# Kernel optimization log

Measured on AMD Instinct MI355X. Metric: run time of the kernel, lower is better.

The kernel has to match this reference:

```python
import jax, jax.numpy as jnp
import numpy as np

N_NODES = 100000
IN_CH = 256
EMBED = 256
N_EDGES = 300000
EPS = 1e-5


def _glorot(key, shape):
    fan_in, fan_out = shape[0], shape[1]
    lim = (6.0 / (fan_in + fan_out)) ** 0.5
    return jax.random.uniform(key, shape, jnp.float32, -lim, lim)


def setup_inputs() -> dict:
    key = jax.random.key(0)
    ks = jax.random.split(key, 16)
    inp = {}
    inp['node_feat'] = jax.random.normal(ks[0], (N_NODES, IN_CH), jnp.float32)
    inp['src'] = jax.random.randint(ks[1], (N_EDGES,), 0, N_NODES, jnp.int32)
    inp['dst'] = jax.random.randint(ks[2], (N_EDGES,), 0, N_NODES, jnp.int32)
    inp['neg'] = jax.random.randint(ks[3], (N_EDGES,), 0, N_NODES, jnp.int32)
    # GCNConv weights (x @ W + b), 3 layers
    inp['W1'] = _glorot(ks[4], (IN_CH, EMBED)); inp['b1'] = jnp.zeros((EMBED,), jnp.float32)
    inp['W2'] = _glorot(ks[5], (EMBED, EMBED)); inp['b2'] = jnp.zeros((EMBED,), jnp.float32)
    inp['W3'] = _glorot(ks[6], (EMBED, EMBED)); inp['b3'] = jnp.zeros((EMBED,), jnp.float32)
    # BatchNorm affine params (2 BN layers)
    inp['g1'] = jnp.ones((EMBED,), jnp.float32); inp['be1'] = jnp.zeros((EMBED,), jnp.float32)
    inp['g2'] = jnp.ones((EMBED,), jnp.float32); inp['be2'] = jnp.zeros((EMBED,), jnp.float32)
    # LinkPredictor MLP
    inp['fc1_w'] = _glorot(ks[7], (2 * EMBED, EMBED)); inp['fc1_b'] = jnp.zeros((EMBED,), jnp.float32)
    inp['fc2_w'] = _glorot(ks[8], (EMBED, 1)); inp['fc2_b'] = jnp.zeros((1,), jnp.float32)
    return inp


def gcn_conv(x, W, b, src, dst, n):
    # PyG GCNConv: out = D^{-1/2} (A + I) D^{-1/2} (x @ W) + b
    xw = x @ W
    loops = jnp.arange(n, dtype=src.dtype)
    src_l = jnp.concatenate([src, loops])
    dst_l = jnp.concatenate([dst, loops])
    deg = jax.ops.segment_sum(jnp.ones_like(dst_l, jnp.float32), dst_l, num_segments=n)
    dinv = jnp.where(deg > 0, jax.lax.rsqrt(deg), 0.0)
    norm = dinv[src_l] * dinv[dst_l]  # [E+N]
    msg = norm[:, None] * xw[src_l]   # [E+N, d]
    out = jax.ops.segment_sum(msg, dst_l, num_segments=n)
    return out + b


def batch_norm(x, g, b):
    # training-mode BN over node dim, biased variance (torch semantics)
    mu = jnp.mean(x, axis=0)
    var = jnp.mean((x - mu) ** 2, axis=0)
    return (x - mu) * jax.lax.rsqrt(var + EPS) * g + b


def link_pred(z_a, z_b, fc1_w, fc1_b, fc2_w, fc2_b):
    h = jnp.concatenate([z_a, z_b], axis=1) @ fc1_w + fc1_b
    h = jax.nn.relu(h)
    return jax.nn.sigmoid(h @ fc2_w + fc2_b).reshape(-1)


def reference(node_feat, src, dst, neg, W1, b1, W2, b2, W3, b3, g1, be1, g2, be2, fc1_w, fc1_b, fc2_w, fc2_b):
    n = node_feat.shape[0]
    # encoder (dropout p used only in training; inference/deterministic here)
    x = gcn_conv(node_feat, W1, b1, src, dst, n)
    x = jax.nn.relu(batch_norm(x, g1, be1))
    x = gcn_conv(x, W2, b2, src, dst, n)
    x = jax.nn.relu(batch_norm(x, g2, be2))
    z = gcn_conv(x, W3, b3, src, dst, n)
    z_src, z_dst, z_neg = z[src], z[dst], z[neg]
    pos_out = link_pred(z_src, z_dst, fc1_w, fc1_b, fc2_w, fc2_b)
    neg_out = link_pred(z_src, z_neg, fc1_w, fc1_b, fc2_w, fc2_b)
    return (pos_out, neg_out)
```

## Files before the change

kernel.cpp:

```cpp
#include <hip/hip_runtime.h>
#include <hip/hip_bf16.h>

#define N_NODES 100000
#define N_EDGES 300000
#define CH 256
#define EPS 1e-5f
#define AGG_BLOCKS 3125
#define Y_TILES 782
#define Y_TILES_PAD 784

typedef __hip_bfloat16 bf16;
typedef __attribute__((ext_vector_type(8))) short bf16x8_t;
typedef __attribute__((ext_vector_type(4))) float f32x4_t;

__device__ __forceinline__ unsigned short f2bf(float f) {
    bf16 h = __float2bfloat16(f);
    return __builtin_bit_cast(unsigned short, h);
}
__device__ __forceinline__ float bf2f(unsigned short u) {
    unsigned int x = ((unsigned int)u) << 16;
    return __builtin_bit_cast(float, x);
}
__device__ __forceinline__ float bflo(unsigned int w) {
    return __builtin_bit_cast(float, w << 16);
}
__device__ __forceinline__ float bfhi(unsigned int w) {
    return __builtin_bit_cast(float, w & 0xffff0000u);
}
__device__ __forceinline__ unsigned pack2(float a, float b) {
    return (unsigned)f2bf(a) | ((unsigned)f2bf(b) << 16);
}
__device__ __forceinline__ void store_val(bf16* p, float v) { *p = __float2bfloat16(v); }

__device__ __forceinline__ void async_copy16(const void* g, void* l) {
    __builtin_amdgcn_global_load_lds((const __attribute__((address_space(1))) void*)g,
                                     (__attribute__((address_space(3))) void*)l, 16, 0, 0);
}

__global__ void k_zero_int(int* __restrict__ p, int n) {
    int i = blockIdx.x * 256 + threadIdx.x;
    if (i < n) p[i] = 0;
}
__global__ void k_count_deg(const int* __restrict__ dst, int* __restrict__ deg) {
    int e = blockIdx.x * 256 + threadIdx.x;
    if (e < N_EDGES) atomicAdd(&deg[dst[e]], 1);
}
__global__ void k_dinv_from_deg(const int* __restrict__ deg, float* __restrict__ dinv) {
    int i = blockIdx.x * 256 + threadIdx.x;
    if (i < N_NODES) dinv[i] = rsqrtf((float)(deg[i] + 1));
}
__global__ void k_block_sums(const int* __restrict__ deg, int* __restrict__ bsum) {
    __shared__ int s[256];
    int t = threadIdx.x;
    int i = blockIdx.x * 256 + t;
    s[t] = (i < N_NODES) ? deg[i] : 0;
    __syncthreads();
    for (int off = 128; off > 0; off >>= 1) {
        if (t < off) s[t] += s[t + off];
        __syncthreads();
    }
    if (t == 0) bsum[blockIdx.x] = s[0];
}
__global__ void k_scan_bsums(int* __restrict__ bsum, int nb) {
    __shared__ int s[512];
    int t = threadIdx.x;
    int v = (t < nb) ? bsum[t] : 0;
    s[t] = v;
    __syncthreads();
    for (int off = 1; off < 512; off <<= 1) {
        int u = (t >= off) ? s[t - off] : 0;
        __syncthreads();
        s[t] += u;
        __syncthreads();
    }
    if (t < nb) bsum[t] = s[t] - v;
}
__global__ void k_row_ptr(const int* __restrict__ deg, const int* __restrict__ bsum,
                          int* __restrict__ row_ptr) {
    __shared__ int s[256];
    int t = threadIdx.x;
    int i = blockIdx.x * 256 + t;
    int v = (i < N_NODES) ? deg[i] : 0;
    s[t] = v;
    __syncthreads();
    for (int off = 1; off < 256; off <<= 1) {
        int u = (t >= off) ? s[t - off] : 0;
        __syncthreads();
        s[t] += u;
        __syncthreads();
    }
    if (i < N_NODES) row_ptr[i] = bsum[blockIdx.x] + s[t] - v;
    if (blockIdx.x == 0 && t == 0) row_ptr[N_NODES] = N_EDGES;
}
__global__ void k_scatter(const int* __restrict__ src, const int* __restrict__ dst,
                          const int* __restrict__ row_ptr, int* __restrict__ cursor,
                          const float* __restrict__ dinv,
                          int* __restrict__ col, float* __restrict__ wedge) {
    int e = blockIdx.x * 256 + threadIdx.x;
    if (e < N_EDGES) {
        int d = dst[e], s = src[e];
        int p = atomicAdd(&cursor[d], 1);
        int idx = row_ptr[d] + p;
        col[idx] = s;
        wedge[idx] = dinv[d] * dinv[s];
    }
}

__global__ void k_transpose_all(const float* __restrict__ W1, const float* __restrict__ W2,
                                const float* __restrict__ W3, const float* __restrict__ fc1w,
                                bf16* __restrict__ wt) {
    int which = blockIdx.x >> 8;
    int idx = ((blockIdx.x & 255) << 8) + threadIdx.x;
    int n = idx >> 8, k = idx & 255;
    const float* W; int ro = 0;
    switch (which) {
        case 0: W = W1; break;
        case 1: W = W2; break;
        case 2: W = W3; break;
        case 3: W = fc1w; break;
        default: W = fc1w; ro = 256; break;
    }
    wt[(size_t)which * 65536 + (size_t)n * 256 + k] =
        __float2bfloat16(W[(size_t)(ro + k) * 256 + n]);
}

__global__ void k_cast_bf16_v4(const float* __restrict__ x, unsigned short* __restrict__ y) {
    int i = blockIdx.x * 256 + threadIdx.x;
    float4 v = ((const float4*)x)[i];
    ushort4 o;
    o.x = f2bf(v.x); o.y = f2bf(v.y); o.z = f2bf(v.z); o.w = f2bf(v.w);
    ((ushort4*)y)[i] = o;
}
__global__ void k_bn_relu_bf16(unsigned short* __restrict__ x, const float* __restrict__ scale,
                               const float* __restrict__ shift) {
    int i = blockIdx.x * 256 + threadIdx.x;
    ushort4 m = ((ushort4*)x)[i];
    int c = (i & 63) * 4;
    float4 sc = *(const float4*)(scale + c);
    float4 sh = *(const float4*)(shift + c);
    ushort4 o;
    o.x = f2bf(fmaxf(bf2f(m.x) * sc.x + sh.x, 0.f));
    o.y = f2bf(fmaxf(bf2f(m.y) * sc.y + sh.y, 0.f));
    o.z = f2bf(fmaxf(bf2f(m.z) * sc.z + sh.z, 0.f));
    o.w = f2bf(fmaxf(bf2f(m.w) * sc.w + sh.w, 0.f));
    ((ushort4*)x)[i] = o;
}

template <int NX, bool BIAS>
__global__ __launch_bounds__(256) void k_gemm_mfma(const bf16* __restrict__ A,
                                                   const bf16* __restrict__ Bt,
                                                   bf16* __restrict__ C, int M, int ldc,
                                                   const float* __restrict__ bias256) {
    constexpr int LOG2NX = (NX == 4) ? 2 : 1;
    int id = blockIdx.x;
    int rg = (id & 7) + 8 * (id >> (3 + LOG2NX));
    int ct = (id >> 3) & (NX - 1);
    if (rg >= Y_TILES) return;
    const int row0 = rg * 128;
    const int col0 = ct * 128;

    __shared__ bf16 As[128 * 64];
    __shared__ bf16 Bs[128 * 64];
    const int tid = threadIdx.x;
    const int lane = tid & 63;
    const int w = tid >> 6;
    const int wr = w >> 1, wc = w & 1;
    const int lr = lane & 15, quad = lane >> 4;

    f32x4_t acc[4][4] = {};

    for (int k0 = 0; k0 < 256; k0 += 64) {
#pragma unroll
        for (int i = 0; i < 4; ++i) {
            int j = i * 256 + tid;
            int r = j >> 3, c = j & 7;
            int gk = ((c ^ (r & 7)) << 3);
            int gr = row0 + r; gr = gr < M ? gr : M - 1;
            async_copy16(A + (size_t)gr * 256 + k0 + gk, (void*)(As + j * 8));
            async_copy16(Bt + (size_t)(col0 + r) * 256 + k0 + gk, (void*)(Bs + j * 8));
        }
        __syncthreads();
#pragma unroll
        for (int ks = 0; ks < 2; ++ks) {
            bf16x8_t af[4], bfr[4];
#pragma unroll
            for (int mi = 0; mi < 4; ++mi) {
                int m = wr * 64 + mi * 16 + lr;
                int c = (ks * 4 + quad) ^ (m & 7);
                af[mi] = *(const bf16x8_t*)(As + m * 64 + c * 8);
            }
#pragma unroll
            for (int ni = 0; ni < 4; ++ni) {
                int n = wc * 64 + ni * 16 + lr;
                int c = (ks * 4 + quad) ^ (n & 7);
                bfr[ni] = *(const bf16x8_t*)(Bs + n * 64 + c * 8);
            }
#pragma unroll
            for (int mi = 0; mi < 4; ++mi)
#pragma unroll
                for (int ni = 0; ni < 4; ++ni)
                    acc[mi][ni] = __builtin_amdgcn_mfma_f32_16x16x32_bf16(
                        af[mi], bfr[ni], acc[mi][ni], 0, 0, 0);
        }
        __syncthreads();
    }
    float bv[4];
#pragma unroll
    for (int ni = 0; ni < 4; ++ni) {
        int colg = col0 + wc * 64 + ni * 16 + lr;
        bv[ni] = (BIAS && colg < 256) ? bias256[colg] : 0.f;
    }
#pragma unroll
    for (int mi = 0; mi < 4; ++mi) {
#pragma unroll
        for (int r = 0; r < 4; ++r) {
            int row = row0 + wr * 64 + mi * 16 + quad * 4 + r;
            if (row < M) {
#pragma unroll
                for (int ni = 0; ni < 4; ++ni) {
                    int colg = col0 + wc * 64 + ni * 16 + lr;
                    store_val(C + (size_t)row * ldc + colg, acc[mi][ni][r] + bv[ni]);
                }
            }
        }
    }
}

template <bool STATS>
__global__ __launch_bounds__(256) void k_agg_csr(const unsigned short* __restrict__ xw,
                                                 const int* __restrict__ row_ptr,
                                                 const int* __restrict__ col,
                                                 const float* __restrict__ wedge,
                                                 const float* __restrict__ dinv,
                                                 const float* __restrict__ bias,
                                                 bf16* __restrict__ out,
                                                 float* __restrict__ part) {
    __shared__ float sred[8][256];
    __shared__ float qred[8][256];
    int g = threadIdx.x >> 5, lh = threadIdx.x & 31;
    int base = blockIdx.x * 32 + g * 4;
    const uint4* xwv = (const uint4*)xw;
    float4 b0 = ((const float4*)bias)[lh * 2];
    float4 b1 = ((const float4*)bias)[lh * 2 + 1];
    float s8[8] = {}, q8[8] = {};
#pragma unroll
    for (int n = 0; n < 4; ++n) {
        int node = base + n;
        int beg = row_ptr[node], end = row_ptr[node + 1];
        float dv = dinv[node];
        uint4 xr = xwv[(size_t)node * 32 + lh];
        float s2 = dv * dv;
        float a0 = s2 * bflo(xr.x), a1 = s2 * bfhi(xr.x);
        float a2 = s2 * bflo(xr.y), a3 = s2 * bfhi(xr.y);
        float a4 = s2 * bflo(xr.z), a5 = s2 * bfhi(xr.z);
        float a6 = s2 * bflo(xr.w), a7 = s2 * bfhi(xr.w);
        int i = beg;
        for (; i + 2 <= end; i += 2) {
            int sa = col[i], sb = col[i + 1];
            float wa = wedge[i], wb = wedge[i + 1];
            uint4 ma = xwv[(size_t)sa * 32 + lh];
            uint4 mb = xwv[(size_t)sb * 32 + lh];
            a0 += wa * bflo(ma.x) + wb * bflo(mb.x);
            a1 += wa * bfhi(ma.x) + wb * bfhi(mb.x);
            a2 += wa * bflo(ma.y) + wb * bflo(mb.y);
            a3 += wa * bfhi(ma.y) + wb * bfhi(mb.y);
            a4 += wa * bflo(ma.z) + wb * bflo(mb.z);
            a5 += wa * bfhi(ma.z) + wb * bfhi(mb.z);
            a6 += wa * bflo(ma.w) + wb * bflo(mb.w);
            a7 += wa * bfhi(ma.w) + wb * bfhi(mb.w);
        }
        if (i < end) {
            int sa = col[i];
            float wa = wedge[i];
            uint4 ma = xwv[(size_t)sa * 32 + lh];
            a0 += wa * bflo(ma.x); a1 += wa * bfhi(ma.x);
            a2 += wa * bflo(ma.y); a3 += wa * bfhi(ma.y);
            a4 += wa * bflo(ma.z); a5 += wa * bfhi(ma.z);
            a6 += wa * bflo(ma.w); a7 += wa * bfhi(ma.w);
        }
        a0 += b0.x; a1 += b0.y; a2 += b0.z; a3 += b0.w;
        a4 += b1.x; a5 += b1.y; a6 += b1.z; a7 += b1.w;
        uint4 o;
        o.x = pack2(a0, a1); o.y = pack2(a2, a3);
        o.z = pack2(a4, a5); o.w = pack2(a6, a7);
        ((uint4*)(out + (size_t)node * CH))[lh] = o;
        if (STATS) {
            s8[0] += a0; s8[1] += a1; s8[2] += a2; s8[3] += a3;
            s8[4] += a4; s8[5] += a5; s8[6] += a6; s8[7] += a7;
            q8[0] += a0 * a0; q8[1] += a1 * a1; q8[2] += a2 * a2; q8[3] += a3 * a3;
            q8[4] += a4 * a4; q8[5] += a5 * a5; q8[6] += a6 * a6; q8[7] += a7 * a7;
        }
    }
    if (STATS) {
#pragma unroll
        for (int j = 0; j < 8; ++j) {
            sred[g][lh * 8 + j] = s8[j];
            qred[g][lh * 8 + j] = q8[j];
        }
        __syncthreads();
        int t = threadIdx.x;
        float ss = 0.f, qq = 0.f;
#pragma unroll
        for (int gg = 0; gg < 8; ++gg) {
            ss += sred[gg][t];
            qq += qred[gg][t];
        }
        part[(size_t)blockIdx.x * 512 + t] = ss;
        part[(size_t)blockIdx.x * 512 + 256 + t] = qq;
    }
}

__global__ __launch_bounds__(256) void k_bn_finalize(const float* __restrict__ part,
                                                     const float* __restrict__ g,
                                                     const float* __restrict__ be,
                                                     float* __restrict__ scale,
                                                     float* __restrict__ shift) {
    int wave = threadIdx.x >> 6, lane = threadIdx.x & 63;
    int c = blockIdx.x * 4 + wave;
    float s = 0.f, q = 0.f;
    for (int j = lane; j < AGG_BLOCKS; j += 64) {
        s += part[(size_t)j * 512 + c];
        q += part[(size_t)j * 512 + 256 + c];
    }
#pragma unroll
    for (int off = 32; off > 0; off >>= 1) {
        s += __shfl_down(s, off, 64);
        q += __shfl_down(q, off, 64);
    }
    if (lane == 0) {
        float mu = s * (1.0f / N_NODES);
        float var = q * (1.0f / N_NODES) - mu * mu;
        float sc = g[c] * rsqrtf(var + EPS);
        scale[c] = sc;
        shift[c] = be[c] - mu * sc;
    }
}

__global__ __launch_bounds__(256) void k_edge_score(
        const unsigned short* __restrict__ uv,
        const int* __restrict__ src, const int* __restrict__ dst,
        const int* __restrict__ neg,
        const float* __restrict__ fc2_w, const float* __restrict__ fc2_b,
        float* __restrict__ out) {
    int wave = threadIdx.x >> 6, lane = threadIdx.x & 63;
    int qtr = lane >> 4, l = lane & 15;
    int e = blockIdx.x * 16 + wave * 4 + qtr;
    if (e >= N_EDGES) return;
    int s = src[e], d = dst[e], g = neg[e];
    const uint4* uvv = (const uint4*)uv;
    uint4 u0 = uvv[(size_t)s * 64 + l * 2];
    uint4 u1 = uvv[(size_t)s * 64 + l * 2 + 1];
    uint4 p0 = uvv[(size_t)d * 64 + 32 + l * 2];
    uint4 p1 = uvv[(size_t)d * 64 + 32 + l * 2 + 1];
    uint4 n0 = uvv[(size_t)g * 64 + 32 + l * 2];
    uint4 n1 = uvv[(size_t)g * 64 + 32 + l * 2 + 1];
    float4 w0 = ((const float4*)fc2_w)[l * 4];
    float4 w1 = ((const float4*)fc2_w)[l * 4 + 1];
    float4 w2 = ((const float4*)fc2_w)[l * 4 + 2];
    float4 w3 = ((const float4*)fc2_w)[l * 4 + 3];

    float t0 = bflo(u0.x), t1 = bfhi(u0.x), t2 = bflo(u0.y), t3 = bfhi(u0.y);
    float t4 = bflo(u0.z), t5 = bfhi(u0.z), t6 = bflo(u0.w), t7 = bfhi(u0.w);
    float t8 = bflo(u1.x), t9 = bfhi(u1.x), ta = bflo(u1.y), tb = bfhi(u1.y);
    float tc = bflo(u1.z), td = bfhi(u1.z), te = bflo(u1.w), tf = bfhi(u1.w);

    float accp =
        fmaxf(t0 + bflo(p0.x), 0.f) * w0.x + fmaxf(t1 + bfhi(p0.x), 0.f) * w0.y +
        fmaxf(t2 + bflo(p0.y), 0.f) * w0.z + fmaxf(t3 + bfhi(p0.y), 0.f) * w0.w +
        fmaxf(t4 + bflo(p0.z), 0.f) * w1.x + fmaxf(t5 + bfhi(p0.z), 0.f) * w1.y +
        fmaxf(t6 + bflo(p0.w), 0.f) * w1.z + fmaxf(t7 + bfhi(p0.w), 0.f) * w1.w +
        fmaxf(t8 + bflo(p1.x), 0.f) * w2.x + fmaxf(t9 + bfhi(p1.x), 0.f) * w2.y +
        fmaxf(ta + bflo(p1.y), 0.f) * w2.z + fmaxf(tb + bfhi(p1.y), 0.f) * w2.w +
        fmaxf(tc + bflo(p1.z), 0.f) * w3.x + fmaxf(td + bfhi(p1.z), 0.f) * w3.y +
        fmaxf(te + bflo(p1.w), 0.f) * w3.z + fmaxf(tf + bfhi(p1.w), 0.f) * w3.w;
    float accn =
        fmaxf(t0 + bflo(n0.x), 0.f) * w0.x + fmaxf(t1 + bfhi(n0.x), 0.f) * w0.y +
        fmaxf(t2 + bflo(n0.y), 0.f) * w0.z + fmaxf(t3 + bfhi(n0.y), 0.f) * w0.w +
        fmaxf(t4 + bflo(n0.z), 0.f) * w1.x + fmaxf(t5 + bfhi(n0.z), 0.f) * w1.y +
        fmaxf(t6 + bflo(n0.w), 0.f) * w1.z + fmaxf(t7 + bfhi(n0.w), 0.f) * w1.w +
        fmaxf(t8 + bflo(n1.x), 0.f) * w2.x + fmaxf(t9 + bfhi(n1.x), 0.f) * w2.y +
        fmaxf(ta + bflo(n1.y), 0.f) * w2.z + fmaxf(tb + bfhi(n1.y), 0.f) * w2.w +
        fmaxf(tc + bflo(n1.z), 0.f) * w3.x + fmaxf(td + bfhi(n1.z), 0.f) * w3.y +
        fmaxf(te + bflo(n1.w), 0.f) * w3.z + fmaxf(tf + bfhi(n1.w), 0.f) * w3.w;
#pragma unroll
    for (int off = 8; off > 0; off >>= 1) {
        accp += __shfl_down(accp, off, 64);
        accn += __shfl_down(accn, off, 64);
    }
    if (l == 0) {
        float bb = fc2_b[0];
        out[e] = 1.0f / (1.0f + expf(-(accp + bb)));
        out[N_EDGES + e] = 1.0f / (1.0f + expf(-(accn + bb)));
    }
}

extern "C" void kernel_launch(void* const* d_in, const int* in_sizes, int n_in,
                              void* d_out, int out_size, void* d_ws, size_t ws_size,
                              hipStream_t stream) {
    const float* node_feat = (const float*)d_in[0];
    const int* src = (const int*)d_in[1];
    const int* dst = (const int*)d_in[2];
    const int* neg = (const int*)d_in[3];
    const float* W1 = (const float*)d_in[4];  const float* b1 = (const float*)d_in[5];
    const float* W2 = (const float*)d_in[6];  const float* b2 = (const float*)d_in[7];
    const float* W3 = (const float*)d_in[8];  const float* b3 = (const float*)d_in[9];
    const float* g1 = (const float*)d_in[10]; const float* be1 = (const float*)d_in[11];
    const float* g2 = (const float*)d_in[12]; const float* be2 = (const float*)d_in[13];
    const float* fc1_w = (const float*)d_in[14]; const float* fc1_b = (const float*)d_in[15];
    const float* fc2_w = (const float*)d_in[16]; const float* fc2_b = (const float*)d_in[17];
    float* out = (float*)d_out;

    const size_t NF = (size_t)N_NODES * CH;
    bf16* UV = (bf16*)d_ws;
    bf16* Xbf = UV + 2 * NF;
    bf16* XwBf = Xbf + NF;
    bf16* wt = XwBf + NF;
    float* dinv = (float*)(wt + 5 * 65536);
    float* bnpart = dinv + N_NODES;
    float* scale = bnpart + (size_t)AGG_BLOCKS * 512;
    float* shift = scale + CH;
    float* wedge = shift + CH;
    int* ideg = (int*)(wedge + N_EDGES);
    int* cursor = ideg + N_NODES;
    int* row_ptr = cursor + N_NODES;
    int* col = row_ptr + N_NODES + 1;
    int* bsum = col + N_EDGES;
    (void)ws_size;

    int gemmBlocks = 2 * Y_TILES_PAD;
    int uvBlocks = 4 * Y_TILES_PAD;
    int nodeBlocks = (N_NODES + 255) / 256;
    int edgeBlocks = (N_EDGES + 255) / 256;
    int v4Blocks = (int)(NF / 4 / 256);
    int scoreBlocks = (N_EDGES + 15) / 16;

    k_zero_int<<<(2 * N_NODES + 255) / 256, 256, 0, stream>>>(ideg, 2 * N_NODES);
    k_count_deg<<<edgeBlocks, 256, 0, stream>>>(dst, ideg);
    k_dinv_from_deg<<<nodeBlocks, 256, 0, stream>>>(ideg, dinv);
    k_block_sums<<<nodeBlocks, 256, 0, stream>>>(ideg, bsum);
    k_scan_bsums<<<1, 512, 0, stream>>>(bsum, nodeBlocks);
    k_row_ptr<<<nodeBlocks, 256, 0, stream>>>(ideg, bsum, row_ptr);
    k_scatter<<<edgeBlocks, 256, 0, stream>>>(src, dst, row_ptr, cursor, dinv, col, wedge);

    k_transpose_all<<<1280, 256, 0, stream>>>(W1, W2, W3, fc1_w, wt);

    k_cast_bf16_v4<<<v4Blocks, 256, 0, stream>>>(node_feat, (unsigned short*)Xbf);
    k_gemm_mfma<2, false><<<gemmBlocks, 256, 0, stream>>>(Xbf, wt, XwBf, N_NODES, 256, nullptr);
    k_agg_csr<true><<<AGG_BLOCKS, 256, 0, stream>>>((unsigned short*)XwBf, row_ptr, col,
                                                    wedge, dinv, b1, Xbf, bnpart);
    k_bn_finalize<<<64, 256, 0, stream>>>(bnpart, g1, be1, scale, shift);
    k_bn_relu_bf16<<<v4Blocks, 256, 0, stream>>>((unsigned short*)Xbf, scale, shift);

    k_gemm_mfma<2, false><<<gemmBlocks, 256, 0, stream>>>(Xbf, wt + 65536, XwBf, N_NODES, 256, nullptr);
    k_agg_csr<true><<<AGG_BLOCKS, 256, 0, stream>>>((unsigned short*)XwBf, row_ptr, col,
                                                    wedge, dinv, b2, Xbf, bnpart);
    k_bn_finalize<<<64, 256, 0, stream>>>(bnpart, g2, be2, scale, shift);
    k_bn_relu_bf16<<<v4Blocks, 256, 0, stream>>>((unsigned short*)Xbf, scale, shift);

    k_gemm_mfma<2, false><<<gemmBlocks, 256, 0, stream>>>(Xbf, wt + 2 * 65536, XwBf, N_NODES, 256, nullptr);
    k_agg_csr<false><<<AGG_BLOCKS, 256, 0, stream>>>((unsigned short*)XwBf, row_ptr, col,
                                                     wedge, dinv, b3, Xbf, nullptr);

    k_gemm_mfma<4, true><<<uvBlocks, 256, 0, stream>>>(Xbf, wt + 3 * 65536, UV, N_NODES, 512, fc1_b);
    k_edge_score<<<scoreBlocks, 256, 0, stream>>>((unsigned short*)UV, src, dst, neg,
                                                  fc2_w, fc2_b, out);
}
```

Measured before the change: 614.6 us.

## Process edge scores in CSR dst-sorted order with XCD-aware block swizzle

The edge scoring kernel now walks edges in the dst-sorted CSR order, using new eid/rowid arrays written during scatter. It also remaps block IDs so that consecutive chunks land on the same XCD. Together these aim to improve L2 reuse of the dst rows of UV, since edges that share a destination become adjacent. The cost is two extra int arrays written in scatter and an extra indirection to recover the edge id for neg and for the output index. The kernel also now assumes N_EDGES is divisible by 16.

```diff
diff --git a/kernel.cpp b/kernel.cpp
--- a/kernel.cpp
+++ b/kernel.cpp
@@ -95,7 +95,8 @@
 __global__ void k_scatter(const int* __restrict__ src, const int* __restrict__ dst,
                           const int* __restrict__ row_ptr, int* __restrict__ cursor,
                           const float* __restrict__ dinv,
-                          int* __restrict__ col, float* __restrict__ wedge) {
+                          int* __restrict__ col, float* __restrict__ wedge,
+                          int* __restrict__ eid, int* __restrict__ rowid) {
     int e = blockIdx.x * 256 + threadIdx.x;
     if (e < N_EDGES) {
         int d = dst[e], s = src[e];
@@ -103,6 +104,8 @@
         int idx = row_ptr[d] + p;
         col[idx] = s;
         wedge[idx] = dinv[d] * dinv[s];
+        eid[idx] = e;
+        rowid[idx] = d;
     }
 }
 
@@ -338,22 +341,27 @@
 
 __global__ __launch_bounds__(256) void k_edge_score(
         const unsigned short* __restrict__ uv,
-        const int* __restrict__ src, const int* __restrict__ dst,
-        const int* __restrict__ neg,
+        const int* __restrict__ col, const int* __restrict__ eid,
+        const int* __restrict__ rowid, const int* __restrict__ neg,
         const float* __restrict__ fc2_w, const float* __restrict__ fc2_b,
         float* __restrict__ out) {
+    constexpr int NWG = 18750;
+    constexpr int Q = NWG / 8, R = NWG % 8;
+    int bid = blockIdx.x;
+    int xcd = bid & 7, ord = bid >> 3;
+    int swz = ((xcd < R) ? xcd * (Q + 1) : R * (Q + 1) + (xcd - R) * Q) + ord;
     int wave = threadIdx.x >> 6, lane = threadIdx.x & 63;
     int qtr = lane >> 4, l = lane & 15;
-    int e = blockIdx.x * 16 + wave * 4 + qtr;
-    if (e >= N_EDGES) return;
-    int s = src[e], d = dst[e], g = neg[e];
+    int i = swz * 16 + wave * 4 + qtr;
+    int s = col[i], d = rowid[i], e = eid[i];
+    int g = neg[e];
     const uint4* uvv = (const uint4*)uv;
     uint4 u0 = uvv[(size_t)s * 64 + l * 2];
     uint4 u1 = uvv[(size_t)s * 64 + l * 2 + 1];
     uint4 p0 = uvv[(size_t)d * 64 + 32 + l * 2];
-    uint4 p1 = uvv[(size_t)d * 64 + 32 + l * 2 + 1];
+    uint4 p1 = uvv[(size_t)d * 64 + 33 + l * 2];
     uint4 n0 = uvv[(size_t)g * 64 + 32 + l * 2];
-    uint4 n1 = uvv[(size_t)g * 64 + 32 + l * 2 + 1];
+    uint4 n1 = uvv[(size_t)g * 64 + 33 + l * 2];
     float4 w0 = ((const float4*)fc2_w)[l * 4];
     float4 w1 = ((const float4*)fc2_w)[l * 4 + 1];
     float4 w2 = ((const float4*)fc2_w)[l * 4 + 2];
@@ -424,7 +432,9 @@
     int* cursor = ideg + N_NODES;
     int* row_ptr = cursor + N_NODES;
     int* col = row_ptr + N_NODES + 1;
-    int* bsum = col + N_EDGES;
+    int* eid = col + N_EDGES;
+    int* rowid = eid + N_EDGES;
+    int* bsum = rowid + N_EDGES;
     (void)ws_size;
 
     int gemmBlocks = 2 * Y_TILES_PAD;
@@ -432,7 +442,7 @@
     int nodeBlocks = (N_NODES + 255) / 256;
     int edgeBlocks = (N_EDGES + 255) / 256;
     int v4Blocks = (int)(NF / 4 / 256);
-    int scoreBlocks = (N_EDGES + 15) / 16;
+    int scoreBlocks = N_EDGES / 16;
 
     k_zero_int<<<(2 * N_NODES + 255) / 256, 256, 0, stream>>>(ideg, 2 * N_NODES);
     k_count_deg<<<edgeBlocks, 256, 0, stream>>>(dst, ideg);
@@ -440,7 +450,8 @@
     k_block_sums<<<nodeBlocks, 256, 0, stream>>>(ideg, bsum);
     k_scan_bsums<<<1, 512, 0, stream>>>(bsum, nodeBlocks);
     k_row_ptr<<<nodeBlocks, 256, 0, stream>>>(ideg, bsum, row_ptr);
-    k_scatter<<<edgeBlocks, 256, 0, stream>>>(src, dst, row_ptr, cursor, dinv, col, wedge);
+    k_scatter<<<edgeBlocks, 256, 0, stream>>>(src, dst, row_ptr, cursor, dinv, col, wedge,
+                                              eid, rowid);
 
     k_transpose_all<<<1280, 256, 0, stream>>>(W1, W2, W3, fc1_w, wt);
 
@@ -462,6 +473,6 @@
                                                      wedge, dinv, b3, Xbf, nullptr);
 
     k_gemm_mfma<4, true><<<uvBlocks, 256, 0, stream>>>(Xbf, wt + 3 * 65536, UV, N_NODES, 512, fc1_b);
-    k_edge_score<<<scoreBlocks, 256, 0, stream>>>((unsigned short*)UV, src, dst, neg,
+    k_edge_score<<<scoreBlocks, 256, 0, stream>>>((unsigned short*)UV, col, eid, rowid, neg,
                                                   fc2_w, fc2_b, out);
 }
```

Result: slower. 632.5 us (+2.9%).
